# Kernel tuning notes

Hardware: AMD Instinct MI355X
Metric: run time of the kernel (lower is better)

## Reference

```python
import jax, jax.numpy as jnp
import numpy as np

H = 16  # num_heads
D = 1024  # hidden_size

def setup_inputs() -> dict:
    key = jax.random.key(0)
    ks = jax.random.split(key, 9)
    s = 1.0 / np.sqrt(D).astype(np.float32)
    return {
        'x':  jax.random.normal(ks[0], (2, 2048, D), dtype=jnp.float32),
        'wq': jax.random.normal(ks[1], (D, D), dtype=jnp.float32) * s,
        'bq': jax.random.normal(ks[2], (D,), dtype=jnp.float32) * s,
        'wk': jax.random.normal(ks[3], (D, D), dtype=jnp.float32) * s,
        'bk': jax.random.normal(ks[4], (D,), dtype=jnp.float32) * s,
        'wv': jax.random.normal(ks[5], (D, D), dtype=jnp.float32) * s,
        'bv': jax.random.normal(ks[6], (D,), dtype=jnp.float32) * s,
        'wo': jax.random.normal(ks[7], (D, D), dtype=jnp.float32) * s,
        'bo': jax.random.normal(ks[8], (D,), dtype=jnp.float32) * s,
    }

def _split_heads(t):
    # [b, s, (h d)] -> [b, h, s, d]
    b, s, _ = t.shape
    return t.reshape(b, s, H, D // H).transpose(0, 2, 1, 3)

def reference(x, wq, bq, wk, bk, wv, bv, wo, bo):
    q = _split_heads(x @ wq + bq)  # [b, h, s, d]
    k = _split_heads(x @ wk + bk)
    v = _split_heads(x @ wv + bv)
    scale = 1.0 / jnp.sqrt(jnp.asarray(q.shape[-1], q.dtype))
    attn = jnp.einsum('bhqd,bhkd->bhqk', q, k) * scale
    attn = jax.nn.softmax(attn, axis=-1)
    o = jnp.einsum('bhqk,bhkd->bhqd', attn, v)
    b, h, s, d = o.shape
    o = o.transpose(0, 2, 1, 3).reshape(b, s, h * d)  # concat heads
    return o @ wo + bo
```

## Files before the change

### kernel.cpp

```cpp
#include <hip/hip_runtime.h>
#include <stdint.h>
#include <stddef.h>


typedef __bf16 bf16_t;
typedef __bf16 bf16x8 __attribute__((ext_vector_type(8)));
typedef __bf16 bf16x4 __attribute__((ext_vector_type(4)));
typedef __bf16 bf16x2 __attribute__((ext_vector_type(2)));
typedef float  f32x4  __attribute__((ext_vector_type(4)));
typedef float  f32x16 __attribute__((ext_vector_type(16)));
typedef uint32_t u32x4 __attribute__((ext_vector_type(4)));

static constexpr float kQScale = 0.18033688011112042f;

__device__ __forceinline__ void gload_lds16(const bf16_t* g, bf16_t* l) {
  __builtin_amdgcn_global_load_lds((__attribute__((address_space(1))) void*)(void*)g,
                                   (__attribute__((address_space(3))) void*)l, 16, 0, 0);
}

__device__ __forceinline__ uint32_t pk_bf16(float lo, float hi) {
  bf16x2 v; v[0] = (bf16_t)lo; v[1] = (bf16_t)hi;
  return __builtin_bit_cast(uint32_t, v);
}

__global__ __launch_bounds__(256) void prep_k(
    const float* __restrict__ x, bf16_t* __restrict__ xb,
    const float* __restrict__ wq, const float* __restrict__ wk,
    const float* __restrict__ wv, const float* __restrict__ wo,
    bf16_t* __restrict__ wqkvT, bf16_t* __restrict__ woT) {
  __shared__ float t[64][65];
  const int z = blockIdx.z;
  if (z == 4) {
    const int blk = blockIdx.y * 16 + blockIdx.x;
#pragma unroll
    for (int c = 0; c < 16; ++c) {
      const int i = c * 65536 + blk * 256 + threadIdx.x;
      float4 v = ((const float4*)x)[i];
      bf16x4 o;
      o[0] = (bf16_t)v.x; o[1] = (bf16_t)v.y; o[2] = (bf16_t)v.z; o[3] = (bf16_t)v.w;
      ((bf16x4*)xb)[i] = o;
    }
    return;
  }
  const float* src = z == 0 ? wq : z == 1 ? wk : z == 2 ? wv : wo;
  bf16_t* dst = z < 3 ? wqkvT + (size_t)z * 1024 * 1024 : woT;
  int n0 = blockIdx.x * 64, k0 = blockIdx.y * 64;
  int c = threadIdx.x & 63, r4 = threadIdx.x >> 6;
#pragma unroll
  for (int i = 0; i < 16; ++i) {
    int r = r4 + i * 4;
    t[r][c] = src[(size_t)(k0 + r) * 1024 + (n0 + c)];
  }
  __syncthreads();
#pragma unroll
  for (int i = 0; i < 16; ++i) {
    int r = r4 + i * 4;
    dst[(size_t)(n0 + r) * 1024 + (k0 + c)] = (bf16_t)t[c][r];
  }
}

__global__ __launch_bounds__(256) void gemm_qkv_k(
    const bf16_t* __restrict__ A, const bf16_t* __restrict__ Bw,
    bf16_t* __restrict__ Qb, bf16_t* __restrict__ Kb, bf16_t* __restrict__ Vt,
    const float* __restrict__ bq, const float* __restrict__ bk, const float* __restrict__ bv) {
  __shared__ alignas(16) bf16_t As[128 * 32];
  __shared__ alignas(16) bf16_t Bs[128 * 32];
  const int tid = threadIdx.x;
  const int lane = tid & 63;
  const int w = tid >> 6, wr = w >> 1, wc = w & 1;
  const int brow = blockIdx.y * 128, bcol = blockIdx.x * 128;
  const int l15 = lane & 15, ko = (lane >> 4) * 8;

  f32x4 acc[4][4] = {};
  const bf16_t* Ab = A + (size_t)brow * 1024;
  const bf16_t* Bb = Bw + (size_t)bcol * 1024;

  const int e0 = tid * 8;
  const int r0 = e0 >> 5, c0 = e0 & 31;

  for (int k0 = 0; k0 < 1024; k0 += 32) {
    gload_lds16(Ab + (size_t)r0 * 1024 + k0 + c0, &As[e0]);
    gload_lds16(Ab + (size_t)(r0 + 64) * 1024 + k0 + c0, &As[e0 + 2048]);
    gload_lds16(Bb + (size_t)r0 * 1024 + k0 + c0, &Bs[e0]);
    gload_lds16(Bb + (size_t)(r0 + 64) * 1024 + k0 + c0, &Bs[e0 + 2048]);
    __syncthreads();
    bf16x8 af[4], bfg[4];
#pragma unroll
    for (int i = 0; i < 4; ++i)
      af[i] = *(const bf16x8*)&As[(wr * 64 + i * 16 + l15) * 32 + ko];
#pragma unroll
    for (int i = 0; i < 4; ++i)
      bfg[i] = *(const bf16x8*)&Bs[(wc * 64 + i * 16 + l15) * 32 + ko];
#pragma unroll
    for (int i = 0; i < 4; ++i)
#pragma unroll
      for (int j = 0; j < 4; ++j)
        acc[i][j] = __builtin_amdgcn_mfma_f32_16x16x32_bf16(af[i], bfg[j], acc[i][j], 0, 0, 0);
    __syncthreads();
  }

  const int mat = bcol >> 10;
#pragma unroll
  for (int i = 0; i < 4; ++i) {
    const int gm0 = brow + wr * 64 + i * 16 + ((lane >> 4) << 2);
    const int b = gm0 >> 11, s0 = gm0 & 2047;
#pragma unroll
    for (int j = 0; j < 4; ++j) {
      const int gn = bcol + wc * 64 + j * 16 + l15;
      const int col = gn & 1023;
      const int h = col >> 6, dd = col & 63;
      if (mat == 2) {
        const float bsv = bv[col];
        bf16x4 pk;
#pragma unroll
        for (int r = 0; r < 4; ++r) pk[r] = (bf16_t)(acc[i][j][r] + bsv);
        *(bf16x4*)&Vt[(((size_t)b * 16 + h) * 64 + dd) * 2048 + s0] = pk;
      } else {
        bf16_t* dst = mat == 0 ? Qb : Kb;
        const float bsv = (mat == 0 ? bq : bk)[col];
        const float scl = mat == 0 ? kQScale : 1.0f;
#pragma unroll
        for (int r = 0; r < 4; ++r)
          dst[((((size_t)b * 16 + h) * 2048 + (s0 + r)) * 64 + dd)] = (bf16_t)((acc[i][j][r] + bsv) * scl);
      }
    }
  }
}

__global__ __launch_bounds__(256) void gemm_out_k(
    const bf16_t* __restrict__ A, const bf16_t* __restrict__ Bw,
    float* __restrict__ outF, const float* __restrict__ bo) {
  __shared__ alignas(16) bf16_t As[128 * 32];
  __shared__ alignas(16) bf16_t Bs[64 * 32];
  const int tid = threadIdx.x;
  const int lane = tid & 63;
  const int w = tid >> 6;
  const int brow = blockIdx.y * 128, bcol = blockIdx.x * 64;
  const int l15 = lane & 15, ko = (lane >> 4) * 8;

  f32x4 acc[2][4] = {};
  const bf16_t* Ab = A + (size_t)brow * 1024;
  const bf16_t* Bb = Bw + (size_t)bcol * 1024;

  const int e0 = tid * 8;
  const int r0 = e0 >> 5, c0 = e0 & 31;

  for (int k0 = 0; k0 < 1024; k0 += 32) {
    gload_lds16(Ab + (size_t)r0 * 1024 + k0 + c0, &As[e0]);
    gload_lds16(Ab + (size_t)(r0 + 64) * 1024 + k0 + c0, &As[e0 + 2048]);
    gload_lds16(Bb + (size_t)r0 * 1024 + k0 + c0, &Bs[e0]);
    __syncthreads();
    bf16x8 af[2], bfg[4];
#pragma unroll
    for (int i = 0; i < 2; ++i)
      af[i] = *(const bf16x8*)&As[(w * 32 + i * 16 + l15) * 32 + ko];
#pragma unroll
    for (int j = 0; j < 4; ++j)
      bfg[j] = *(const bf16x8*)&Bs[(j * 16 + l15) * 32 + ko];
#pragma unroll
    for (int i = 0; i < 2; ++i)
#pragma unroll
      for (int j = 0; j < 4; ++j)
        acc[i][j] = __builtin_amdgcn_mfma_f32_16x16x32_bf16(af[i], bfg[j], acc[i][j], 0, 0, 0);
    __syncthreads();
  }

#pragma unroll
  for (int i = 0; i < 2; ++i) {
    const int gm0 = brow + w * 32 + i * 16 + ((lane >> 4) << 2);
#pragma unroll
    for (int j = 0; j < 4; ++j) {
      const int gn = bcol + j * 16 + l15;
      const float bsv = bo[gn];
#pragma unroll
      for (int r = 0; r < 4; ++r)
        outF[(size_t)(gm0 + r) * 1024 + gn] = acc[i][j][r] + bsv;
    }
  }
}

__global__ __launch_bounds__(256, 2) void attn_k(
    const bf16_t* __restrict__ Qb, const bf16_t* __restrict__ Kb,
    const bf16_t* __restrict__ Vt, bf16_t* __restrict__ O) {
  __shared__ alignas(16) bf16_t Ksm[2][4096];
  __shared__ alignas(16) bf16_t Vsm[2][4096];
  const int tid = threadIdx.x, lane = tid & 63, w = tid >> 6;
  const int l31 = lane & 31, hi = lane >> 5;
  const int work = (blockIdx.x & 7) * 64 + (blockIdx.x >> 3);
  const int bh = work >> 4;
  const int q0 = (work & 15) * 128 + w * 32;

  const bf16_t* Qp = Qb + ((size_t)bh * 2048 + q0) * 64;

  const int chunk0 = w * 64 + lane;
  const int srow = chunk0 >> 3;
  const int swzc = (chunk0 & 7) ^ (srow & 7);
  const char* srcK0 = (const char*)(Kb + (size_t)bh * 2048 * 64) + srow * 128 + swzc * 16;
  const char* srcK1 = srcK0 + 32 * 128;
  const char* srcV0 = (const char*)(Vt + (size_t)bh * 64 * 2048) + srow * 4096 + swzc * 16;
  const char* srcV1 = srcV0 + 32 * 4096;

  auto stage = [&](int buf) {
    bf16_t* kb = &Ksm[buf][w * 512];
    bf16_t* vb = &Vsm[buf][w * 512];
    gload_lds16((const bf16_t*)srcK0, kb);
    gload_lds16((const bf16_t*)srcK1, kb + 2048);
    gload_lds16((const bf16_t*)srcV0, vb);
    gload_lds16((const bf16_t*)srcV1, vb + 2048);
    srcK0 += 8192; srcK1 += 8192;
    srcV0 += 128;  srcV1 += 128;
  };

  const int xorv = l31 & 7;
  const bf16_t* kcb[4];
  const bf16_t* vcb[4];
#pragma unroll
  for (int j = 0; j < 4; ++j) {
    const int co = ((j * 2 + hi) ^ xorv) * 8;
    kcb[j] = &Ksm[0][l31 * 64 + co];
    vcb[j] = &Vsm[0][l31 * 64 + co];
  }

  bf16x8 qf[4];
#pragma unroll
  for (int ds = 0; ds < 4; ++ds)
    qf[ds] = *(const bf16x8*)&Qp[(size_t)l31 * 64 + ds * 16 + hi * 8];

  f32x16 o0 = {}, o1 = {};
  float mx = -1e30f, li = 0.0f;

  auto tile_body = [&](int buf) {
    const int bo = buf * 4096;
    bf16x8 kf0[4], kf1[4];
#pragma unroll
    for (int ds = 0; ds < 4; ++ds) {
      kf0[ds] = *(const bf16x8*)(kcb[ds] + bo);
      kf1[ds] = *(const bf16x8*)(kcb[ds] + bo + 2048);
    }
    f32x16 s0 = {}, s1 = {};
    __builtin_amdgcn_s_setprio(1);
#pragma unroll
    for (int ds = 0; ds < 4; ++ds)
      s0 = __builtin_amdgcn_mfma_f32_32x32x16_bf16(kf0[ds], qf[ds], s0, 0, 0, 0);
#pragma unroll
    for (int ds = 0; ds < 4; ++ds)
      s1 = __builtin_amdgcn_mfma_f32_32x32x16_bf16(kf1[ds], qf[ds], s1, 0, 0, 0);
    __builtin_amdgcn_s_setprio(0);
    bf16x8 vf0[4], vf1[4];
#pragma unroll
    for (int ks = 0; ks < 4; ++ks) {
      vf0[ks] = *(const bf16x8*)(vcb[ks] + bo);
      vf1[ks] = *(const bf16x8*)(vcb[ks] + bo + 2048);
    }

    float m8[8];
#pragma unroll
    for (int r = 0; r < 8; ++r)
      m8[r] = fmaxf(fmaxf(s0[r], s0[r + 8]), fmaxf(s1[r], s1[r + 8]));
    float m4a = fmaxf(m8[0], m8[4]), m4b = fmaxf(m8[1], m8[5]);
    float m4c = fmaxf(m8[2], m8[6]), m4d = fmaxf(m8[3], m8[7]);
    float tmax = fmaxf(fmaxf(m4a, m4b), fmaxf(m4c, m4d));
    tmax = fmaxf(tmax, __shfl_xor(tmax, 32));

    if (__any(tmax > mx + 8.0f)) {
      const float mn = fmaxf(mx, tmax);
      const float corr = __builtin_amdgcn_exp2f(mx - mn);
      mx = mn;
      li *= corr;
#pragma unroll
      for (int r = 0; r < 16; ++r) { o0[r] *= corr; o1[r] *= corr; }
    }

    float ra = 0.f, rb = 0.f, rc = 0.f, rd = 0.f;
#pragma unroll
    for (int r = 0; r < 4; ++r) {
      float p0 = __builtin_amdgcn_exp2f(s0[r] - mx);       s0[r] = p0; ra += p0;
      float p1 = __builtin_amdgcn_exp2f(s0[r + 4] - mx);   s0[r + 4] = p1; rb += p1;
      float p2 = __builtin_amdgcn_exp2f(s0[r + 8] - mx);   s0[r + 8] = p2; rc += p2;
      float p3 = __builtin_amdgcn_exp2f(s0[r + 12] - mx);  s0[r + 12] = p3; rd += p3;
      float p4 = __builtin_amdgcn_exp2f(s1[r] - mx);       s1[r] = p4; ra += p4;
      float p5 = __builtin_amdgcn_exp2f(s1[r + 4] - mx);   s1[r + 4] = p5; rb += p5;
      float p6 = __builtin_amdgcn_exp2f(s1[r + 8] - mx);   s1[r + 8] = p6; rc += p6;
      float p7 = __builtin_amdgcn_exp2f(s1[r + 12] - mx);  s1[r + 12] = p7; rd += p7;
    }
    float rs = (ra + rb) + (rc + rd);
    rs += __shfl_xor(rs, 32);
    li += rs;

    uint32_t pw0[8], pw1[8];
#pragma unroll
    for (int g = 0; g < 4; ++g) {
      pw0[g * 2 + 0] = pk_bf16(s0[4 * g + 0], s0[4 * g + 1]);
      pw0[g * 2 + 1] = pk_bf16(s0[4 * g + 2], s0[4 * g + 3]);
      pw1[g * 2 + 0] = pk_bf16(s1[4 * g + 0], s1[4 * g + 1]);
      pw1[g * 2 + 1] = pk_bf16(s1[4 * g + 2], s1[4 * g + 3]);
    }

#pragma unroll
    for (int st = 0; st < 2; ++st) {
      uint32_t (&pw)[8] = st ? pw1 : pw0;
#pragma unroll
      for (int ks = 0; ks < 2; ++ks) {
        const uint32_t A0 = pw[(2 * ks) * 2 + 0], A1 = pw[(2 * ks) * 2 + 1];
        const uint32_t B0 = pw[(2 * ks + 1) * 2 + 0], B1 = pw[(2 * ks + 1) * 2 + 1];
        const uint32_t Z0 = hi ? A0 : B0;
        const uint32_t Z1 = hi ? A1 : B1;
        const uint32_t sZ0 = (uint32_t)__shfl_xor((int)Z0, 32);
        const uint32_t sZ1 = (uint32_t)__shfl_xor((int)Z1, 32);
        u32x4 fw;
        fw[0] = hi ? sZ0 : A0;
        fw[1] = hi ? sZ1 : A1;
        fw[2] = hi ? B0 : sZ0;
        fw[3] = hi ? B1 : sZ1;
        const bf16x8 pf = __builtin_bit_cast(bf16x8, fw);
        __builtin_amdgcn_s_setprio(1);
        o0 = __builtin_amdgcn_mfma_f32_32x32x16_bf16(vf0[st * 2 + ks], pf, o0, 0, 0, 0);
        o1 = __builtin_amdgcn_mfma_f32_32x32x16_bf16(vf1[st * 2 + ks], pf, o1, 0, 0, 0);
        __builtin_amdgcn_s_setprio(0);
      }
    }
  };

  stage(0);
  __syncthreads();
#pragma unroll 1
  for (int t = 0; t < 32; t += 2) {
    stage(1);
    tile_body(0);
    __syncthreads();
    if (t + 2 < 32) stage(0);
    tile_body(1);
    if (t + 2 < 32) __syncthreads();
  }

  const int b = bh >> 4, h = bh & 15;
  const float inv = 1.0f / li;
  const size_t row = (size_t)b * 2048 + q0 + l31;
#pragma unroll
  for (int g = 0; g < 4; ++g) {
    bf16x4 p0, p1;
#pragma unroll
    for (int r = 0; r < 4; ++r) {
      p0[r] = (bf16_t)(o0[4 * g + r] * inv);
      p1[r] = (bf16_t)(o1[4 * g + r] * inv);
    }
    *(bf16x4*)&O[row * 1024 + h * 64 + 0  + g * 8 + hi * 4] = p0;
    *(bf16x4*)&O[row * 1024 + h * 64 + 32 + g * 8 + hi * 4] = p1;
  }
}

extern "C" void kernel_launch(void* const* d_in, const int* in_sizes, int n_in,
                              void* d_out, int out_size, void* d_ws, size_t ws_size,
                              hipStream_t stream) {
  const float* x  = (const float*)d_in[0];
  const float* wq = (const float*)d_in[1];
  const float* bq = (const float*)d_in[2];
  const float* wk = (const float*)d_in[3];
  const float* bk = (const float*)d_in[4];
  const float* wv = (const float*)d_in[5];
  const float* bv = (const float*)d_in[6];
  const float* wo = (const float*)d_in[7];
  const float* bo = (const float*)d_in[8];
  float* out = (float*)d_out;

  if (ws_size < ((size_t)48 << 20)) return;
  char* ws = (char*)d_ws;
  bf16_t* xb  = (bf16_t*)(ws);
  bf16_t* wT  = (bf16_t*)(ws + ((size_t)8 << 20));
  bf16_t* woT = wT + (size_t)3072 * 1024;
  bf16_t* Qb  = (bf16_t*)(ws + ((size_t)16 << 20));
  bf16_t* Kb  = (bf16_t*)(ws + ((size_t)24 << 20));
  bf16_t* Vt  = (bf16_t*)(ws + ((size_t)32 << 20));
  bf16_t* O   = xb;

  prep_k<<<dim3(16, 16, 5), 256, 0, stream>>>(x, xb, wq, wk, wv, wo, wT, woT);
  gemm_qkv_k<<<dim3(24, 32), 256, 0, stream>>>(xb, wT, Qb, Kb, Vt, bq, bk, bv);
  attn_k<<<512, 256, 0, stream>>>(Qb, Kb, Vt, O);
  gemm_out_k<<<dim3(16, 32), 256, 0, stream>>>(O, woT, out, bo);
}
```

Before: 122.7 us.

## Split key range across two warp groups per attention block and merge in LDS

Doubles the attention block to 512 threads, with two groups of four warps each handling half of the key/value sequence for the same 128 queries. After the loop, one half writes its partial output, max and sum to shared memory, and the other rescales and combines them before writing the bf16 output. This raises wave count per CU to hide load and MFMA latency better. In exchange it adds a merge phase, doubles shared memory use and tightens the register budget under the new launch bounds.

```diff
diff --git a/kernel.cpp b/kernel.cpp
--- a/kernel.cpp
+++ b/kernel.cpp
@@ -179,30 +179,31 @@
   }
 }
 
-__global__ __launch_bounds__(256, 2) void attn_k(
+__global__ __launch_bounds__(512, 2) void attn_k(
     const bf16_t* __restrict__ Qb, const bf16_t* __restrict__ Kb,
     const bf16_t* __restrict__ Vt, bf16_t* __restrict__ O) {
-  __shared__ alignas(16) bf16_t Ksm[2][4096];
-  __shared__ alignas(16) bf16_t Vsm[2][4096];
+  __shared__ alignas(16) bf16_t Ksm[2][2][4096];
+  __shared__ alignas(16) bf16_t Vsm[2][2][4096];
   const int tid = threadIdx.x, lane = tid & 63, w = tid >> 6;
   const int l31 = lane & 31, hi = lane >> 5;
+  const int qsub = w & 3, half = w >> 2;
   const int work = (blockIdx.x & 7) * 64 + (blockIdx.x >> 3);
   const int bh = work >> 4;
-  const int q0 = (work & 15) * 128 + w * 32;
+  const int q0 = (work & 15) * 128 + qsub * 32;
 
   const bf16_t* Qp = Qb + ((size_t)bh * 2048 + q0) * 64;
 
-  const int chunk0 = w * 64 + lane;
+  const int chunk0 = qsub * 64 + lane;
   const int srow = chunk0 >> 3;
   const int swzc = (chunk0 & 7) ^ (srow & 7);
-  const char* srcK0 = (const char*)(Kb + (size_t)bh * 2048 * 64) + srow * 128 + swzc * 16;
+  const char* srcK0 = (const char*)(Kb + ((size_t)bh * 2048 + half * 1024) * 64) + srow * 128 + swzc * 16;
   const char* srcK1 = srcK0 + 32 * 128;
-  const char* srcV0 = (const char*)(Vt + (size_t)bh * 64 * 2048) + srow * 4096 + swzc * 16;
+  const char* srcV0 = (const char*)(Vt + (size_t)bh * 64 * 2048 + half * 1024) + srow * 4096 + swzc * 16;
   const char* srcV1 = srcV0 + 32 * 4096;
 
   auto stage = [&](int buf) {
-    bf16_t* kb = &Ksm[buf][w * 512];
-    bf16_t* vb = &Vsm[buf][w * 512];
+    bf16_t* kb = &Ksm[half][buf][qsub * 512];
+    bf16_t* vb = &Vsm[half][buf][qsub * 512];
     gload_lds16((const bf16_t*)srcK0, kb);
     gload_lds16((const bf16_t*)srcK1, kb + 2048);
     gload_lds16((const bf16_t*)srcV0, vb);
@@ -217,8 +218,8 @@
 #pragma unroll
   for (int j = 0; j < 4; ++j) {
     const int co = ((j * 2 + hi) ^ xorv) * 8;
-    kcb[j] = &Ksm[0][l31 * 64 + co];
-    vcb[j] = &Vsm[0][l31 * 64 + co];
+    kcb[j] = &Ksm[half][0][l31 * 64 + co];
+    vcb[j] = &Vsm[half][0][l31 * 64 + co];
   }
 
   bf16x8 qf[4];
@@ -324,28 +325,51 @@
   stage(0);
   __syncthreads();
 #pragma unroll 1
-  for (int t = 0; t < 32; t += 2) {
+  for (int t = 0; t < 16; t += 2) {
     stage(1);
     tile_body(0);
     __syncthreads();
-    if (t + 2 < 32) stage(0);
+    if (t + 2 < 16) stage(0);
     tile_body(1);
-    if (t + 2 < 32) __syncthreads();
-  }
-
-  const int b = bh >> 4, h = bh & 15;
-  const float inv = 1.0f / li;
-  const size_t row = (size_t)b * 2048 + q0 + l31;
-#pragma unroll
-  for (int g = 0; g < 4; ++g) {
-    bf16x4 p0, p1;
-#pragma unroll
-    for (int r = 0; r < 4; ++r) {
-      p0[r] = (bf16_t)(o0[4 * g + r] * inv);
-      p1[r] = (bf16_t)(o1[4 * g + r] * inv);
-    }
-    *(bf16x4*)&O[row * 1024 + h * 64 + 0  + g * 8 + hi * 4] = p0;
-    *(bf16x4*)&O[row * 1024 + h * 64 + 32 + g * 8 + hi * 4] = p1;
+    if (t + 2 < 16) __syncthreads();
+  }
+
+  __syncthreads();
+  float* cmb_o = (float*)&Ksm[0][0][0];
+  float* cmb_m = (float*)&Vsm[0][0][0];
+  float* cmb_l = cmb_m + 256;
+  if (half) {
+    cmb_m[qsub * 64 + lane] = mx;
+    cmb_l[qsub * 64 + lane] = li;
+#pragma unroll
+    for (int r = 0; r < 16; ++r) {
+      cmb_o[(qsub * 32 + r) * 64 + lane] = o0[r];
+      cmb_o[(qsub * 32 + 16 + r) * 64 + lane] = o1[r];
+    }
+  }
+  __syncthreads();
+  if (!half) {
+    const float mb = cmb_m[qsub * 64 + lane];
+    const float lb = cmb_l[qsub * 64 + lane];
+    const float M = fmaxf(mx, mb);
+    const float ca = __builtin_amdgcn_exp2f(mx - M);
+    const float cb = __builtin_amdgcn_exp2f(mb - M);
+    const float L = li * ca + lb * cb;
+    const float inv = 1.0f / L;
+    const float fa = ca * inv, fb = cb * inv;
+    const int b = bh >> 4, h = bh & 15;
+    const size_t row = (size_t)b * 2048 + q0 + l31;
+#pragma unroll
+    for (int g = 0; g < 4; ++g) {
+      bf16x4 p0, p1;
+#pragma unroll
+      for (int r = 0; r < 4; ++r) {
+        p0[r] = (bf16_t)(o0[4 * g + r] * fa + cmb_o[(qsub * 32 + 4 * g + r) * 64 + lane] * fb);
+        p1[r] = (bf16_t)(o1[4 * g + r] * fa + cmb_o[(qsub * 32 + 16 + 4 * g + r) * 64 + lane] * fb);
+      }
+      *(bf16x4*)&O[row * 1024 + h * 64 + 0  + g * 8 + hi * 4] = p0;
+      *(bf16x4*)&O[row * 1024 + h * 64 + 32 + g * 8 + hi * 4] = p1;
+    }
   }
 }
 
@@ -375,6 +399,6 @@
 
   prep_k<<<dim3(16, 16, 5), 256, 0, stream>>>(x, xb, wq, wk, wv, wo, wT, woT);
   gemm_qkv_k<<<dim3(24, 32), 256, 0, stream>>>(xb, wT, Qb, Kb, Vt, bq, bk, bv);
-  attn_k<<<512, 256, 0, stream>>>(Qb, Kb, Vt, O);
+  attn_k<<<512, 512, 0, stream>>>(Qb, Kb, Vt, O);
   gemm_out_k<<<dim3(16, 32), 256, 0, stream>>>(O, woT, out, bo);
 }
```

Measured after the change: 123.7 us. About the same (+0.9%).
